# Optimization experiments

Hardware: AMD Instinct MI355X
Metric: run time of the kernel (lower is better)

The kernel has to match this reference:

```python
import jax, jax.numpy as jnp
import numpy as np

N_VERTS = 1_000_000
N_JOINTS = 55  # SMPL-X: NUM_JOINTS + 1


def setup_inputs() -> dict:
    key = jax.random.key(0)
    k1, k2, k3 = jax.random.split(key, 3)
    points = jax.random.normal(k1, (N_VERTS, 3), dtype=jnp.float32)
    w = jax.random.uniform(k2, (N_VERTS, N_JOINTS), dtype=jnp.float32)
    weights = w / jnp.sum(w, axis=-1, keepdims=True)  # LBS weights sum to 1 per vertex
    SE3 = jax.random.normal(k3, (N_JOINTS, 4, 4), dtype=jnp.float32)
    return {"points": points, "weights": weights, "SE3": SE3}


def reference(points, weights, SE3):
    # RigidTransform.weight: blend per-joint SE(3) matrices with per-vertex weights
    # weights: [N, J], SE3: [J, 4, 4] -> A: [N, 4, 4]
    A = jnp.einsum('nj,jkl->nkl', weights, SE3)
    R = A[:, :3, :3]  # [N, 3, 3]
    T = A[:, :3, 3]   # [N, 3]
    # RigidTransform._transform_points: R @ p + T
    return jnp.einsum('nkl,nl->nk', R, points) + T
```

## Files before the change

kernel.cpp:

```cpp
#include <hip/hip_runtime.h>

#define NJ   55
#define BLK  64
#define SLABF (BLK * NJ)
#define STG  14

__global__ __launch_bounds__(BLK, 3) void lbs_kernel(
    const float* __restrict__ points,
    const float* __restrict__ weights,
    const float* __restrict__ se3,
    float* __restrict__ out,
    int n_verts, int n_slabs, int gstride)
{
    __shared__ __align__(16) float s_w[SLABF];
    const int lane = threadIdx.x;

    int s = blockIdx.x;
    if (s >= n_slabs) return;

    {
        const int rows = min(BLK, n_verts - s * BLK);
        if (rows == BLK) {
            const float4* src = (const float4*)(weights + (size_t)s * SLABF);
            float4* dst = (float4*)s_w;
            #pragma unroll
            for (int i = 0; i < STG - 1; ++i) dst[lane + i * BLK] = src[lane + i * BLK];
            if (lane < 48) dst[lane + (STG - 1) * BLK] = src[lane + (STG - 1) * BLK];
        } else {
            const float* src = weights + (size_t)s * SLABF;
            for (int i = lane; i < rows * NJ; i += BLK) s_w[i] = src[i];
        }
    }

    for (;;) {
        const int snext = s + gstride;
        const bool have_next = (snext < n_slabs);

        const int n = s * BLK + lane;
        const bool act = (n < n_verts);
        const int nc = act ? n : (n_verts - 1);

        const float px = points[nc * 3 + 0];
        const float py = points[nc * 3 + 1];
        const float pz = points[nc * 3 + 2];

        float4 stg[STG];
        bool full_next = false;
        if (have_next) {
            const int rows = min(BLK, n_verts - snext * BLK);
            full_next = (rows == BLK);
            if (full_next) {
                const float4* src = (const float4*)(weights + (size_t)snext * SLABF);
                #pragma unroll
                for (int i = 0; i < STG - 1; ++i) stg[i] = src[lane + i * BLK];
                if (lane < 48) stg[STG - 1] = src[lane + (STG - 1) * BLK];
            }
        }

        float a[12];
        #pragma unroll
        for (int e = 0; e < 12; ++e) a[e] = 0.f;

        const float* wr = &s_w[lane * NJ];
        const float4* M = (const float4*)se3;

        #pragma unroll 5
        for (int j = 0; j < NJ; ++j) {
            const float w = wr[j];
            const float4 r0 = M[j * 4 + 0];
            const float4 r1 = M[j * 4 + 1];
            const float4 r2 = M[j * 4 + 2];
            a[0] += w * r0.x; a[1] += w * r0.y; a[2]  += w * r0.z; a[3]  += w * r0.w;
            a[4] += w * r1.x; a[5] += w * r1.y; a[6]  += w * r1.z; a[7]  += w * r1.w;
            a[8] += w * r2.x; a[9] += w * r2.y; a[10] += w * r2.z; a[11] += w * r2.w;
        }

        if (act) {
            float* po = out + (size_t)n * 3;
            po[0] = a[0] * px + a[1] * py + a[2]  * pz + a[3];
            po[1] = a[4] * px + a[5] * py + a[6]  * pz + a[7];
            po[2] = a[8] * px + a[9] * py + a[10] * pz + a[11];
        }

        if (!have_next) return;

        if (full_next) {
            float4* dst = (float4*)s_w;
            #pragma unroll
            for (int i = 0; i < STG - 1; ++i) dst[lane + i * BLK] = stg[i];
            if (lane < 48) dst[lane + (STG - 1) * BLK] = stg[STG - 1];
        } else {
            const int rows = n_verts - snext * BLK;
            const float* src = weights + (size_t)snext * SLABF;
            for (int i = lane; i < rows * NJ; i += BLK) s_w[i] = src[i];
        }
        s = snext;
    }
}

extern "C" void kernel_launch(void* const* d_in, const int* in_sizes, int n_in,
                              void* d_out, int out_size, void* d_ws, size_t ws_size,
                              hipStream_t stream) {
    const float* points  = (const float*)d_in[0];
    const float* weights = (const float*)d_in[1];
    const float* se3     = (const float*)d_in[2];
    float* out = (float*)d_out;

    const int n_verts = in_sizes[0] / 3;
    const int n_slabs = (n_verts + BLK - 1) / BLK;
    int grid = 11 * 256;
    if (grid > n_slabs) grid = n_slabs;
    lbs_kernel<<<grid, BLK, 0, stream>>>(points, weights, se3, out,
                                         n_verts, n_slabs, grid);
}
```

Before: 359.6 us.

## Double-buffer weight slabs in LDS using direct global-to-LDS loads

Replaces the register-staged prefetch of the next weight slab with direct global_load_lds transfers into a second LDS buffer, and swaps the two buffers each iteration. Point coordinates for the next slab are also prefetched. The aim is to free the 14 float4 staging registers and the LDS write pass, so the loads overlap with the FMA loop. The cost is twice the LDS per block and a smaller grid (5*256 instead of 11*256). Occupancy and latency hiding change as a result, and the waitcnt encoding is hardcoded.

```diff
diff --git a/kernel.cpp b/kernel.cpp
--- a/kernel.cpp
+++ b/kernel.cpp
@@ -1,59 +1,75 @@
 #include <hip/hip_runtime.h>
 
-#define NJ   55
-#define BLK  64
+#define NJ    55
+#define BLK   64
 #define SLABF (BLK * NJ)
-#define STG  14
+#define WAIT_VM0 0x0F70
 
-__global__ __launch_bounds__(BLK, 3) void lbs_kernel(
+#define AS_G(p) ((const __attribute__((address_space(1))) void*)(p))
+#define AS_L(p) ((__attribute__((address_space(3))) void*)(p))
+
+__device__ __forceinline__ void dma_slab(const float* __restrict__ src,
+                                         float* dst, int lane) {
+    #pragma unroll
+    for (int i = 0; i < 13; ++i)
+        __builtin_amdgcn_global_load_lds(AS_G(src + i * 256 + lane * 4),
+                                         AS_L(dst + i * 256 + lane * 4), 16, 0, 0);
+    if (lane < 48)
+        __builtin_amdgcn_global_load_lds(AS_G(src + 13 * 256 + lane * 4),
+                                         AS_L(dst + 13 * 256 + lane * 4), 16, 0, 0);
+}
+
+__global__ __launch_bounds__(BLK) void lbs_kernel(
     const float* __restrict__ points,
     const float* __restrict__ weights,
     const float* __restrict__ se3,
     float* __restrict__ out,
     int n_verts, int n_slabs, int gstride)
 {
-    __shared__ __align__(16) float s_w[SLABF];
+    __shared__ __align__(16) float sA[SLABF];
+    __shared__ __align__(16) float sB[SLABF];
+
     const int lane = threadIdx.x;
-
     int s = blockIdx.x;
     if (s >= n_slabs) return;
 
+    float* cur = sA;
+    float* nxt = sB;
+
+    float px, py, pz;
     {
+        const int n = s * BLK + lane;
+        const int nc = (n < n_verts) ? n : (n_verts - 1);
+        px = points[nc * 3 + 0];
+        py = points[nc * 3 + 1];
+        pz = points[nc * 3 + 2];
         const int rows = min(BLK, n_verts - s * BLK);
         if (rows == BLK) {
-            const float4* src = (const float4*)(weights + (size_t)s * SLABF);
-            float4* dst = (float4*)s_w;
-            #pragma unroll
-            for (int i = 0; i < STG - 1; ++i) dst[lane + i * BLK] = src[lane + i * BLK];
-            if (lane < 48) dst[lane + (STG - 1) * BLK] = src[lane + (STG - 1) * BLK];
+            dma_slab(weights + (size_t)s * SLABF, cur, lane);
         } else {
             const float* src = weights + (size_t)s * SLABF;
-            for (int i = lane; i < rows * NJ; i += BLK) s_w[i] = src[i];
+            for (int i = lane; i < rows * NJ; i += BLK) cur[i] = src[i];
         }
+        __builtin_amdgcn_s_waitcnt(WAIT_VM0);
     }
 
     for (;;) {
         const int snext = s + gstride;
         const bool have_next = (snext < n_slabs);
 
-        const int n = s * BLK + lane;
-        const bool act = (n < n_verts);
-        const int nc = act ? n : (n_verts - 1);
-
-        const float px = points[nc * 3 + 0];
-        const float py = points[nc * 3 + 1];
-        const float pz = points[nc * 3 + 2];
-
-        float4 stg[STG];
-        bool full_next = false;
+        float pxn, pyn, pzn;
         if (have_next) {
+            const int n2 = snext * BLK + lane;
+            const int nc2 = (n2 < n_verts) ? n2 : (n_verts - 1);
+            pxn = points[nc2 * 3 + 0];
+            pyn = points[nc2 * 3 + 1];
+            pzn = points[nc2 * 3 + 2];
             const int rows = min(BLK, n_verts - snext * BLK);
-            full_next = (rows == BLK);
-            if (full_next) {
-                const float4* src = (const float4*)(weights + (size_t)snext * SLABF);
-                #pragma unroll
-                for (int i = 0; i < STG - 1; ++i) stg[i] = src[lane + i * BLK];
-                if (lane < 48) stg[STG - 1] = src[lane + (STG - 1) * BLK];
+            if (rows == BLK) {
+                dma_slab(weights + (size_t)snext * SLABF, nxt, lane);
+            } else {
+                const float* src = weights + (size_t)snext * SLABF;
+                for (int i = lane; i < rows * NJ; i += BLK) nxt[i] = src[i];
             }
         }
 
@@ -61,7 +77,7 @@
         #pragma unroll
         for (int e = 0; e < 12; ++e) a[e] = 0.f;
 
-        const float* wr = &s_w[lane * NJ];
+        const float* wr = &cur[lane * NJ];
         const float4* M = (const float4*)se3;
 
         #pragma unroll 5
@@ -75,7 +91,8 @@
             a[8] += w * r2.x; a[9] += w * r2.y; a[10] += w * r2.z; a[11] += w * r2.w;
         }
 
-        if (act) {
+        const int n = s * BLK + lane;
+        if (n < n_verts) {
             float* po = out + (size_t)n * 3;
             po[0] = a[0] * px + a[1] * py + a[2]  * pz + a[3];
             po[1] = a[4] * px + a[5] * py + a[6]  * pz + a[7];
@@ -84,16 +101,9 @@
 
         if (!have_next) return;
 
-        if (full_next) {
-            float4* dst = (float4*)s_w;
-            #pragma unroll
-            for (int i = 0; i < STG - 1; ++i) dst[lane + i * BLK] = stg[i];
-            if (lane < 48) dst[lane + (STG - 1) * BLK] = stg[STG - 1];
-        } else {
-            const int rows = n_verts - snext * BLK;
-            const float* src = weights + (size_t)snext * SLABF;
-            for (int i = lane; i < rows * NJ; i += BLK) s_w[i] = src[i];
-        }
+        __builtin_amdgcn_s_waitcnt(WAIT_VM0);
+        float* t = cur; cur = nxt; nxt = t;
+        px = pxn; py = pyn; pz = pzn;
         s = snext;
     }
 }
@@ -108,7 +118,7 @@
 
     const int n_verts = in_sizes[0] / 3;
     const int n_slabs = (n_verts + BLK - 1) / BLK;
-    int grid = 11 * 256;
+    int grid = 5 * 256;
     if (grid > n_slabs) grid = n_slabs;
     lbs_kernel<<<grid, BLK, 0, stream>>>(points, weights, se3, out,
                                          n_verts, n_slabs, grid);
```

Measured after the change: 318.8 us. 11.4% less time.
